# Performance work log

Measured on AMD Instinct MI355X. Metric: run time of the kernel, lower is better.

The kernel has to match this reference:

```python
import jax, jax.numpy as jnp
import numpy as np

N_NODES = 50000
N_EDGES = 1600000
NFEAT = 128
NHID = 128
NCLASS = 64
BATCH = 8


def setup_inputs() -> dict:
    key = jax.random.key(0)
    ks = jax.random.split(key, 8)
    x = jax.random.normal(ks[0], (BATCH, N_NODES, NFEAT), dtype=jnp.float32)
    edge_rows = jnp.sort(jax.random.randint(ks[1], (N_EDGES,), 0, N_NODES))
    edge_cols = jax.random.randint(ks[2], (N_EDGES,), 0, N_NODES)
    # roughly degree-normalized positive weights (avg degree 32)
    edge_vals = jax.random.uniform(ks[3], (N_EDGES,), dtype=jnp.float32) / 32.0
    s1 = 1.0 / np.sqrt(NFEAT)
    W1 = jax.random.normal(ks[4], (NFEAT, NHID), dtype=jnp.float32) * s1
    W2 = jax.random.normal(ks[5], (NHID, NHID), dtype=jnp.float32) * s1
    W3 = jax.random.normal(ks[6], (NHID, NCLASS), dtype=jnp.float32) * s1
    b1 = jnp.zeros((NHID,), dtype=jnp.float32)
    b2 = jnp.zeros((NHID,), dtype=jnp.float32)
    b3 = jnp.zeros((NCLASS,), dtype=jnp.float32)
    return {"x": x, "edge_rows": edge_rows, "edge_cols": edge_cols,
            "edge_vals": edge_vals, "W1": W1, "b1": b1, "W2": W2,
            "b2": b2, "W3": W3, "b3": b3}


def _gcn_layer(x, W, b, rows, cols, vals, n_nodes):
    """Batched SPGraphConvolution: spmm(adj, x @ W) + b, x: [B, N, d_in]."""
    support = jnp.einsum("bnd,de->bne", x, W)  # [B, N, d_out]

    def spmm(s):  # s: [N, d_out]
        msgs = s[cols] * vals[:, None]  # gather + scale, [E, d_out]
        return jax.ops.segment_sum(msgs, rows, num_segments=n_nodes)

    return jax.vmap(spmm)(support) + b


def reference(x, edge_rows, edge_cols, edge_vals, W1, b1, W2, b2, W3, b3):
    n = x.shape[1]
    # dropout in eval mode (training=False) for determinism
    h = jax.nn.relu(_gcn_layer(x, W1, b1, edge_rows, edge_cols, edge_vals, n) + x)
    h = jax.nn.relu(_gcn_layer(h, W2, b2, edge_rows, edge_cols, edge_vals, n) + h)
    h = jax.nn.relu(_gcn_layer(h, W3, b3, edge_rows, edge_cols, edge_vals, n))
    return jax.nn.sigmoid(h)
```

## Files before the change

### kernel.cpp

```cpp
#include <hip/hip_runtime.h>

constexpr int NN = 50000;
constexpr int NE = 1600000;
constexpr int NB = 8;
constexpr int M_ROWS = NN * NB;

typedef unsigned short ushort;
typedef unsigned int uint;
typedef unsigned char uchar;
typedef float f32x2v __attribute__((ext_vector_type(2)));
typedef float f32x4v __attribute__((ext_vector_type(4)));
typedef uint u32x4 __attribute__((ext_vector_type(4)));
typedef uint u32x2 __attribute__((ext_vector_type(2)));

__device__ __forceinline__ ushort f2bf(float f) {
  union { float f; uint u; } v;
  v.f = f;
  const uint r = v.u + 0x7fffu + ((v.u >> 16) & 1u);
  return (ushort)(r >> 16);
}
__device__ __forceinline__ float bfhi(uint g) {
  union { uint u; float f; } v;
  v.u = g & 0xffff0000u;
  return v.f;
}
__device__ __forceinline__ float bflo(uint g) {
  union { uint u; float f; } v;
  v.u = g << 16;
  return v.f;
}

__device__ __forceinline__ void fp8x4_to_f32x2(uint v, f32x2v& lo, f32x2v& hi) {
#if __has_builtin(__builtin_amdgcn_cvt_pk_f32_fp8)
  lo = __builtin_amdgcn_cvt_pk_f32_fp8((int)v, false);
  hi = __builtin_amdgcn_cvt_pk_f32_fp8((int)v, true);
#else
  union { _Float16 h; ushort u; } c0, c1, c2, c3;
  c0.u = (ushort)(((v & 0x80u) << 8) | ((v & 0x7fu) << 7));
  c1.u = (ushort)(((v & 0x8000u)) | ((v & 0x7f00u) >> 1));
  c2.u = (ushort)((((v >> 16) & 0x80u) << 8) | (((v >> 16) & 0x7fu) << 7));
  c3.u = (ushort)((((v >> 24) & 0x80u) << 8) | (((v >> 24) & 0x7fu) << 7));
  lo.x = (float)c0.h * 256.0f;
  lo.y = (float)c1.h * 256.0f;
  hi.x = (float)c2.h * 256.0f;
  hi.y = (float)c3.h * 256.0f;
#endif
}
__device__ __forceinline__ uint f32_to_fp8(float x) {
#if __has_builtin(__builtin_amdgcn_cvt_pk_fp8_f32)
  return (uint)__builtin_amdgcn_cvt_pk_fp8_f32(x, x, 0, false) & 0xffu;
#else
  union { _Float16 h; ushort u; } c;
  c.h = (_Float16)(x * (1.0f / 256.0f));
  const uint h = c.u;
  uint r = h & 0x7fffu;
  r = (r + 0x3Fu + ((r >> 7) & 1u)) >> 7;
  if (r > 0x7Eu) r = 0x7Eu;
  return ((h >> 8) & 0x80u) | r;
#endif
}

__global__ __launch_bounds__(256) void rowptr_kernel(const int* __restrict__ rows,
                                                     int* __restrict__ row_ptr) {
  const int r = blockIdx.x * 256 + threadIdx.x;
  if (r > NN) return;
  int lo = 0, hi = NE;
  while (lo < hi) {
    const int mid = (lo + hi) >> 1;
    if (rows[mid] < r) lo = mid + 1;
    else hi = mid;
  }
  row_ptr[r] = lo;
}

__global__ __launch_bounds__(256) void wtrans_kernel(const float* __restrict__ W,
                                                     ushort* __restrict__ Wt,
                                                     int dout) {
  const int idx = blockIdx.x * 256 + threadIdx.x;
  if (idx >= dout * 128) return;
  const int n = idx >> 7;
  const int k = idx & 127;
  Wt[idx] = f2bf(W[k * dout + n]);
}

template <int DOUT, bool ABF16>
__global__ __launch_bounds__(256) void gemm_mfma(const void* __restrict__ Av,
                                                 const ushort* __restrict__ Wt,
                                                 uchar* __restrict__ S) {
  constexpr int PACK = 256 / DOUT;
  constexpr int NT = DOUT / 16;
  constexpr int RT = 5;
  constexpr int LDK = 136;
  constexpr int LB = DOUT + 16;
  typedef __attribute__((ext_vector_type(8))) short bf16x8;
  typedef __attribute__((ext_vector_type(4))) float f32x4;

  __shared__ ushort As[64 * LDK];
  __shared__ ushort Ws[DOUT * LDK];

  const int t = threadIdx.x;
  const int w = t >> 6;
  const int l = t & 63;

#pragma unroll
  for (int q = 0; q < (DOUT * 128) / (8 * 256); q++) {
    const int chunk = t + q * 256;
    const int n = chunk >> 4;
    const int off = (chunk & 15) * 8;
    *(uint4*)(Ws + n * LDK + off) = *(const uint4*)(Wt + n * 128 + off);
  }

  const int mrow = w * 16 + (l & 15);
  const int q8 = (l >> 4) * 8;

  for (int rt = 0; rt < RT; rt++) {
    const size_t m0 = (size_t)blockIdx.x * (64 * RT) + (size_t)rt * 64;

    if constexpr (ABF16) {
      const ushort* A = (const ushort*)Av;
#pragma unroll
      for (int q = 0; q < 4; q++) {
        const int chunk = t + q * 256;
        const int row = chunk >> 4;
        const int off = (chunk & 15) * 8;
        *(u32x4*)(As + row * LDK + off) =
            __builtin_nontemporal_load((const u32x4*)(A + (m0 + row) * 128 + off));
      }
    } else {
      const float* A = (const float*)Av;
      const int row = t >> 2;
      const int c0 = (t & 3) * 32;
      const float* src = A + (m0 + row) * 128 + c0;
      ushort* dst = As + row * LDK + c0;
#pragma unroll
      for (int q = 0; q < 8; q++) {
        const f32x4v g = __builtin_nontemporal_load((const f32x4v*)(src + q * 4));
        u32x2 p;
        p.x = (uint)f2bf(g.x) | ((uint)f2bf(g.y) << 16);
        p.y = (uint)f2bf(g.z) | ((uint)f2bf(g.w) << 16);
        *(u32x2*)(dst + q * 4) = p;
      }
    }
    __syncthreads();

    bf16x8 a[4];
    const ushort* ap = As + mrow * LDK + q8;
#pragma unroll
    for (int ks = 0; ks < 4; ks++) a[ks] = *(const bf16x8*)(ap + ks * 32);

    f32x4 acc[NT];
#pragma unroll
    for (int nt = 0; nt < NT; nt++) acc[nt] = (f32x4)0.f;

#pragma unroll
    for (int nt = 0; nt < NT; nt++) {
      const ushort* bp = Ws + (nt * 16 + (l & 15)) * LDK + q8;
#pragma unroll
      for (int ks = 0; ks < 4; ks++) {
        const bf16x8 b = *(const bf16x8*)(bp + ks * 32);
        acc[nt] =
            __builtin_amdgcn_mfma_f32_16x16x32_bf16(a[ks], b, acc[nt], 0, 0, 0);
      }
    }

    __syncthreads();
    uchar* Ab = (uchar*)As;
    const int erow = w * 16 + (l >> 4) * 4;
    const int ecol = l & 15;
#pragma unroll
    for (int nt = 0; nt < NT; nt++)
#pragma unroll
      for (int r = 0; r < 4; r++)
        Ab[(erow + r) * LB + nt * 16 + ecol] = (uchar)f32_to_fp8(acc[nt][r]);
    __syncthreads();

#pragma unroll
    for (int q = 0; q < (64 * DOUT) / (16 * 256); q++) {
      const int chunk = t + q * 256;
      const int row = chunk / (DOUT / 16);
      const int off = (chunk % (DOUT / 16)) * 16;
      const uint4 v = *(const uint4*)(Ab + row * LB + off);
      const int m = (int)m0 + row;
      const int b = m / NN;
      const int n = m - b * NN;
      *(uint4*)(S + ((size_t)(b / PACK) * NN + n) * 256 + (b % PACK) * DOUT + off) = v;
    }
    __syncthreads();
  }
}

template <int PACK, int RMODE, bool SIGMOID, bool OBF16>
__global__ __launch_bounds__(256) void spmm_kernel(
    const uchar* __restrict__ S, const int* __restrict__ row_ptr,
    const int* __restrict__ cols, const float* __restrict__ vals,
    const float* __restrict__ bias, const void* resid, void* out) {
  constexpr int DOUT = 256 / PACK;
  constexpr int LPB = 64 / PACK;

  const int wave = threadIdx.x >> 6;
  const int lane = threadIdx.x & 63;
  const int r = blockIdx.x * 4 + wave;
  const int bg = lane / LPB;
  const int j = (lane % LPB) * 4;
  const int b = blockIdx.y * PACK + bg;
  const uchar* __restrict__ Sg = S + (size_t)blockIdx.y * ((size_t)NN * 256);
  const uint lane4 = (uint)lane << 2;

  f32x2v a01 = {0.f, 0.f};
  f32x2v a23 = {0.f, 0.f};

  const int e0 = row_ptr[r];
  const int e1 = row_ptr[r + 1];

  for (int e = e0; e < e1; e += 64) {
    const int n = min(64, e1 - e);
    uint c8 = 0;
    float wv = 0.f;
    if (lane < n) {
      c8 = (uint)__builtin_nontemporal_load(cols + e + lane) << 8;
      wv = __builtin_nontemporal_load(vals + e + lane);
    }
    int i = 0;
    for (; i + 16 <= n; i += 16) {
      float ww[16];
      uint gg[16];
#pragma unroll
      for (int s = 0; s < 16; s++) {
        const uint off = (uint)__shfl((int)c8, i + s) + lane4;
        ww[s] = __shfl(wv, i + s);
        gg[s] = *(const uint*)(Sg + off);
      }
#pragma unroll
      for (int s = 0; s < 16; s++) {
        f32x2v lo, hi;
        fp8x4_to_f32x2(gg[s], lo, hi);
        const f32x2v w2 = {ww[s], ww[s]};
        a01 = __builtin_elementwise_fma(w2, lo, a01);
        a23 = __builtin_elementwise_fma(w2, hi, a23);
      }
    }
    for (; i + 4 <= n; i += 4) {
      float ww[4];
      uint gg[4];
#pragma unroll
      for (int s = 0; s < 4; s++) {
        const uint off = (uint)__shfl((int)c8, i + s) + lane4;
        ww[s] = __shfl(wv, i + s);
        gg[s] = *(const uint*)(Sg + off);
      }
#pragma unroll
      for (int s = 0; s < 4; s++) {
        f32x2v lo, hi;
        fp8x4_to_f32x2(gg[s], lo, hi);
        const f32x2v w2 = {ww[s], ww[s]};
        a01 = __builtin_elementwise_fma(w2, lo, a01);
        a23 = __builtin_elementwise_fma(w2, hi, a23);
      }
    }
    for (; i < n; i++) {
      const uint off = (uint)__shfl((int)c8, i) + lane4;
      const float wi = __shfl(wv, i);
      const uint g = *(const uint*)(Sg + off);
      f32x2v lo, hi;
      fp8x4_to_f32x2(g, lo, hi);
      const f32x2v w2 = {wi, wi};
      a01 = __builtin_elementwise_fma(w2, lo, a01);
      a23 = __builtin_elementwise_fma(w2, hi, a23);
    }
  }

  float a0 = a01.x, a1 = a01.y, a2 = a23.x, a3 = a23.y;

  const size_t orow = (size_t)(b * NN + r) * DOUT + j;
  const f32x4v bb = *(const f32x4v*)(bias + j);
  a0 += bb.x;
  a1 += bb.y;
  a2 += bb.z;
  a3 += bb.w;
  if constexpr (RMODE == 1) {
    const f32x4v res =
        __builtin_nontemporal_load((const f32x4v*)((const float*)resid + orow));
    a0 += res.x;
    a1 += res.y;
    a2 += res.z;
    a3 += res.w;
  } else if constexpr (RMODE == 2) {
    const u32x2 g =
        __builtin_nontemporal_load((const u32x2*)((const ushort*)resid + orow));
    a0 += bflo(g.x);
    a1 += bfhi(g.x);
    a2 += bflo(g.y);
    a3 += bfhi(g.y);
  }
  a0 = fmaxf(a0, 0.f);
  a1 = fmaxf(a1, 0.f);
  a2 = fmaxf(a2, 0.f);
  a3 = fmaxf(a3, 0.f);
  if constexpr (SIGMOID) {
    a0 = 1.f / (1.f + __expf(-a0));
    a1 = 1.f / (1.f + __expf(-a1));
    a2 = 1.f / (1.f + __expf(-a2));
    a3 = 1.f / (1.f + __expf(-a3));
  }
  if constexpr (OBF16) {
    u32x2 o;
    o.x = (uint)f2bf(a0) | ((uint)f2bf(a1) << 16);
    o.y = (uint)f2bf(a2) | ((uint)f2bf(a3) << 16);
    __builtin_nontemporal_store(o, (u32x2*)((ushort*)out + orow));
  } else {
    f32x4v o;
    o.x = a0;
    o.y = a1;
    o.z = a2;
    o.w = a3;
    __builtin_nontemporal_store(o, (f32x4v*)((float*)out + orow));
  }
}

extern "C" void kernel_launch(void* const* d_in, const int* in_sizes, int n_in,
                              void* d_out, int out_size, void* d_ws, size_t ws_size,
                              hipStream_t stream) {
  const float* x = (const float*)d_in[0];
  const int* erows = (const int*)d_in[1];
  const int* ecols = (const int*)d_in[2];
  const float* evals = (const float*)d_in[3];
  const float* W1 = (const float*)d_in[4];
  const float* b1 = (const float*)d_in[5];
  const float* W2 = (const float*)d_in[6];
  const float* b2 = (const float*)d_in[7];
  const float* W3 = (const float*)d_in[8];
  const float* b3 = (const float*)d_in[9];

  char* ws = (char*)d_ws;
  int* row_ptr = (int*)ws;
  ushort* Wt1 = (ushort*)(ws + 0x40000);
  ushort* Wt2 = (ushort*)(ws + 0x48000);
  ushort* Wt3 = (ushort*)(ws + 0x50000);
  uchar* Sf8 = (uchar*)(ws + 0x60000);
  ushort* H = (ushort*)(ws + 0x60000 + (size_t)M_ROWS * 128);

  rowptr_kernel<<<(NN + 256) / 256, 256, 0, stream>>>(erows, row_ptr);
  wtrans_kernel<<<(128 * 128) / 256, 256, 0, stream>>>(W1, Wt1, 128);
  wtrans_kernel<<<(128 * 128) / 256, 256, 0, stream>>>(W2, Wt2, 128);
  wtrans_kernel<<<(64 * 128) / 256, 256, 0, stream>>>(W3, Wt3, 64);

  const dim3 sgrid128(NN / 4, NB / 2);
  const dim3 sgrid64(NN / 4, NB / 4);
  constexpr int GB = M_ROWS / (64 * 5);

  gemm_mfma<128, false><<<GB, 256, 0, stream>>>(x, Wt1, Sf8);
  spmm_kernel<2, 1, false, true><<<sgrid128, 256, 0, stream>>>(
      Sf8, row_ptr, ecols, evals, b1, x, H);
  gemm_mfma<128, true><<<GB, 256, 0, stream>>>(H, Wt2, Sf8);
  spmm_kernel<2, 2, false, true><<<sgrid128, 256, 0, stream>>>(
      Sf8, row_ptr, ecols, evals, b2, H, H);
  gemm_mfma<64, true><<<GB, 256, 0, stream>>>(H, Wt3, Sf8);
  spmm_kernel<4, 0, true, false><<<sgrid64, 256, 0, stream>>>(
      Sf8, row_ptr, ecols, evals, b3, nullptr, (float*)d_out);
}
```

Measured before the change: 942.2 us.

## Keep GEMM operands in registers and drop LDS staging in gemm_mfma

The GEMM kernel now keeps the weight fragments in registers and loads activation fragments straight from global memory into MFMA operands, with no shared-memory tiles. Swapping the MFMA operand order produces a transposed accumulator, so each lane packs four fp8 outputs with the packed convert and writes them directly as one 32-bit nontemporal store. This removes the LDS round trips and all __syncthreads. In exchange, global loads and stores are less coalesced (16-byte loads, 4-byte scattered stores), register pressure is higher, and launch bounds now ask for 2 blocks per CU.

```diff
diff --git a/kernel.cpp b/kernel.cpp
--- a/kernel.cpp
+++ b/kernel.cpp
@@ -59,6 +59,16 @@
   return ((h >> 8) & 0x80u) | r;
 #endif
 }
+__device__ __forceinline__ uint pack4_fp8(float a0, float a1, float a2, float a3) {
+#if __has_builtin(__builtin_amdgcn_cvt_pk_fp8_f32)
+  int u = __builtin_amdgcn_cvt_pk_fp8_f32(a0, a1, 0, false);
+  u = __builtin_amdgcn_cvt_pk_fp8_f32(a2, a3, u, true);
+  return (uint)u;
+#else
+  return f32_to_fp8(a0) | (f32_to_fp8(a1) << 8) | (f32_to_fp8(a2) << 16) |
+         (f32_to_fp8(a3) << 24);
+#endif
+}
 
 __global__ __launch_bounds__(256) void rowptr_kernel(const int* __restrict__ rows,
                                                      int* __restrict__ row_ptr) {
@@ -84,108 +94,75 @@
 }
 
 template <int DOUT, bool ABF16>
-__global__ __launch_bounds__(256) void gemm_mfma(const void* __restrict__ Av,
-                                                 const ushort* __restrict__ Wt,
-                                                 uchar* __restrict__ S) {
+__global__ __launch_bounds__(256, 2) void gemm_mfma(const void* __restrict__ Av,
+                                                    const ushort* __restrict__ Wt,
+                                                    uchar* __restrict__ S) {
   constexpr int PACK = 256 / DOUT;
   constexpr int NT = DOUT / 16;
   constexpr int RT = 5;
-  constexpr int LDK = 136;
-  constexpr int LB = DOUT + 16;
   typedef __attribute__((ext_vector_type(8))) short bf16x8;
   typedef __attribute__((ext_vector_type(4))) float f32x4;
-
-  __shared__ ushort As[64 * LDK];
-  __shared__ ushort Ws[DOUT * LDK];
 
   const int t = threadIdx.x;
   const int w = t >> 6;
   const int l = t & 63;
-
-#pragma unroll
-  for (int q = 0; q < (DOUT * 128) / (8 * 256); q++) {
-    const int chunk = t + q * 256;
-    const int n = chunk >> 4;
-    const int off = (chunk & 15) * 8;
-    *(uint4*)(Ws + n * LDK + off) = *(const uint4*)(Wt + n * 128 + off);
-  }
-
-  const int mrow = w * 16 + (l & 15);
+  const int lr = l & 15;
   const int q8 = (l >> 4) * 8;
+  const int r4 = (l >> 4) * 4;
+
+  bf16x8 wf[NT][4];
+#pragma unroll
+  for (int nt = 0; nt < NT; nt++) {
+    const ushort* wp = Wt + (nt * 16 + lr) * 128 + q8;
+#pragma unroll
+    for (int ks = 0; ks < 4; ks++)
+      wf[nt][ks] = *(const bf16x8*)(wp + ks * 32);
+  }
 
   for (int rt = 0; rt < RT; rt++) {
-    const size_t m0 = (size_t)blockIdx.x * (64 * RT) + (size_t)rt * 64;
-
+    const size_t m = (size_t)blockIdx.x * (64 * RT) + rt * 64 + w * 16 + lr;
+
+    bf16x8 af[4];
     if constexpr (ABF16) {
-      const ushort* A = (const ushort*)Av;
-#pragma unroll
-      for (int q = 0; q < 4; q++) {
-        const int chunk = t + q * 256;
-        const int row = chunk >> 4;
-        const int off = (chunk & 15) * 8;
-        *(u32x4*)(As + row * LDK + off) =
-            __builtin_nontemporal_load((const u32x4*)(A + (m0 + row) * 128 + off));
-      }
+      const ushort* A = (const ushort*)Av + m * 128 + q8;
+#pragma unroll
+      for (int ks = 0; ks < 4; ks++)
+        af[ks] = __builtin_nontemporal_load((const bf16x8*)(A + ks * 32));
     } else {
-      const float* A = (const float*)Av;
-      const int row = t >> 2;
-      const int c0 = (t & 3) * 32;
-      const float* src = A + (m0 + row) * 128 + c0;
-      ushort* dst = As + row * LDK + c0;
-#pragma unroll
-      for (int q = 0; q < 8; q++) {
-        const f32x4v g = __builtin_nontemporal_load((const f32x4v*)(src + q * 4));
-        u32x2 p;
-        p.x = (uint)f2bf(g.x) | ((uint)f2bf(g.y) << 16);
-        p.y = (uint)f2bf(g.z) | ((uint)f2bf(g.w) << 16);
-        *(u32x2*)(dst + q * 4) = p;
-      }
-    }
-    __syncthreads();
-
-    bf16x8 a[4];
-    const ushort* ap = As + mrow * LDK + q8;
-#pragma unroll
-    for (int ks = 0; ks < 4; ks++) a[ks] = *(const bf16x8*)(ap + ks * 32);
+      const float* A = (const float*)Av + m * 128 + q8;
+#pragma unroll
+      for (int ks = 0; ks < 4; ks++) {
+        const f32x4v g0 = __builtin_nontemporal_load((const f32x4v*)(A + ks * 32));
+        const f32x4v g1 =
+            __builtin_nontemporal_load((const f32x4v*)(A + ks * 32 + 4));
+        union { bf16x8 v; u32x4 u; } p;
+        p.u.x = (uint)f2bf(g0.x) | ((uint)f2bf(g0.y) << 16);
+        p.u.y = (uint)f2bf(g0.z) | ((uint)f2bf(g0.w) << 16);
+        p.u.z = (uint)f2bf(g1.x) | ((uint)f2bf(g1.y) << 16);
+        p.u.w = (uint)f2bf(g1.z) | ((uint)f2bf(g1.w) << 16);
+        af[ks] = p.v;
+      }
+    }
 
     f32x4 acc[NT];
 #pragma unroll
     for (int nt = 0; nt < NT; nt++) acc[nt] = (f32x4)0.f;
-
+#pragma unroll
+    for (int nt = 0; nt < NT; nt++)
+#pragma unroll
+      for (int ks = 0; ks < 4; ks++)
+        acc[nt] =
+            __builtin_amdgcn_mfma_f32_16x16x32_bf16(wf[nt][ks], af[ks], acc[nt], 0, 0, 0);
+
+    const int b = (int)(m / NN);
+    const int n_node = (int)(m - (size_t)b * NN);
+    uchar* Srow = S + ((size_t)(b / PACK) * NN + n_node) * 256 +
+                  (b % PACK) * DOUT + r4;
 #pragma unroll
     for (int nt = 0; nt < NT; nt++) {
-      const ushort* bp = Ws + (nt * 16 + (l & 15)) * LDK + q8;
-#pragma unroll
-      for (int ks = 0; ks < 4; ks++) {
-        const bf16x8 b = *(const bf16x8*)(bp + ks * 32);
-        acc[nt] =
-            __builtin_amdgcn_mfma_f32_16x16x32_bf16(a[ks], b, acc[nt], 0, 0, 0);
-      }
-    }
-
-    __syncthreads();
-    uchar* Ab = (uchar*)As;
-    const int erow = w * 16 + (l >> 4) * 4;
-    const int ecol = l & 15;
-#pragma unroll
-    for (int nt = 0; nt < NT; nt++)
-#pragma unroll
-      for (int r = 0; r < 4; r++)
-        Ab[(erow + r) * LB + nt * 16 + ecol] = (uchar)f32_to_fp8(acc[nt][r]);
-    __syncthreads();
-
-#pragma unroll
-    for (int q = 0; q < (64 * DOUT) / (16 * 256); q++) {
-      const int chunk = t + q * 256;
-      const int row = chunk / (DOUT / 16);
-      const int off = (chunk % (DOUT / 16)) * 16;
-      const uint4 v = *(const uint4*)(Ab + row * LB + off);
-      const int m = (int)m0 + row;
-      const int b = m / NN;
-      const int n = m - b * NN;
-      *(uint4*)(S + ((size_t)(b / PACK) * NN + n) * 256 + (b % PACK) * DOUT + off) = v;
-    }
-    __syncthreads();
+      const uint p = pack4_fp8(acc[nt][0], acc[nt][1], acc[nt][2], acc[nt][3]);
+      __builtin_nontemporal_store(p, (uint*)(Srow + nt * 16));
+    }
   }
 }
 
```

Measured after the change: 1.015 ms. 1.08x slower.
